# Kernel tuning notes

Hardware: AMD Instinct MI355X
Metric: run time of the kernel (lower is better)

The kernel has to match this reference:

```python
import jax, jax.numpy as jnp
import numpy as np

N = 100000   # nodes
G = 128      # graphs for mean pool


def gcn_conv(x, edge_index, W, b, num_nodes):
    # PyG GCNConv (default): x' = D^-1/2 (A+I) D^-1/2 (x W) + b
    x = x @ W
    src, dst = edge_index[0], edge_index[1]
    loop = jnp.arange(num_nodes)
    src = jnp.concatenate([src, loop])
    dst = jnp.concatenate([dst, loop])
    ones = jnp.ones(src.shape[0], x.dtype)
    deg = jax.ops.segment_sum(ones, dst, num_segments=num_nodes)
    dinv = jnp.where(deg > 0, jax.lax.rsqrt(deg), 0.0)
    norm = dinv[src] * dinv[dst]            # [E+N]
    msg = x[src] * norm[:, None]            # gather + scale
    out = jax.ops.segment_sum(msg, dst, num_segments=num_nodes)  # scatter-add
    return out + b


def setup_inputs() -> dict:
    key = jax.random.key(0)
    ks = jax.random.split(key, 5)
    x = jax.random.normal(ks[0], (N, 128), jnp.float32)
    edge_index = jax.random.randint(ks[1], (2, 1600000), 0, N)
    batch = jnp.sort(jax.random.randint(ks[2], (N,), 0, G))
    W1 = jax.random.normal(ks[3], (128, 64), jnp.float32) / np.sqrt(128.0)
    b1 = jnp.zeros((64,), jnp.float32)
    W2 = jax.random.normal(ks[4], (64, 64), jnp.float32) / np.sqrt(64.0)
    b2 = jnp.zeros((64,), jnp.float32)
    return {"x": x, "edge_index": edge_index, "batch": batch,
            "W1": W1, "b1": b1, "W2": W2, "b2": b2}


def reference(x, edge_index, batch, W1, b1, W2, b2):
    h = gcn_conv(x, edge_index, W1, b1, N)
    h = jax.nn.relu(h)  # dropout is identity in eval mode
    h = gcn_conv(h, edge_index, W2, b2, N)
    # global_mean_pool over graph ids
    s = jax.ops.segment_sum(h, batch, num_segments=G)
    cnt = jax.ops.segment_sum(jnp.ones((N,), h.dtype), batch, num_segments=G)
    return s / jnp.maximum(cnt, 1.0)[:, None]   # [G, hidden2]
```

## Files before the change

kernel.cpp:

```cpp
#include <hip/hip_runtime.h>
#include <hip/hip_fp16.h>

#define SLOTS 64
#define DEGSTRIDE 16

typedef _Float16 half8 __attribute__((ext_vector_type(8)));
typedef float f32x4 __attribute__((ext_vector_type(4)));

__global__ __launch_bounds__(256) void fill_pad(const int* __restrict__ src,
                                                const int* __restrict__ dst, int E, int N,
                                                int* __restrict__ degp,
                                                int* __restrict__ colpad, int chunks) {
  int range = blockIdx.x & 7;
  int chunk = blockIdx.x >> 3;
  int per = (N + 7) >> 3;
  int lo = range * per, hi = min(N, lo + per);
  int e0 = (int)((long long)chunk * E / chunks);
  int e1 = (int)((long long)(chunk + 1) * E / chunks);
  for (int e = e0 + (int)threadIdx.x; e < e1; e += 256) {
    int d = dst[e];
    if (d >= lo && d < hi) {
      int p = atomicAdd(&degp[(size_t)d * DEGSTRIDE], 1);
      if (p < SLOTS) colpad[(size_t)d * SLOTS + p] = src[e];
    }
  }
}

__global__ __launch_bounds__(256) void calc_dinv(const int* __restrict__ degp,
                                                 float* __restrict__ dinv,
                                                 int* __restrict__ degc, int N) {
  int i = blockIdx.x * 256 + threadIdx.x;
  if (i < N) {
    int d = degp[(size_t)i * DEGSTRIDE];
    dinv[i] = rsqrtf((float)(d + 1));
    degc[i] = min(d, SLOTS);
  }
}

template <int K, typename Tin>
__global__ __launch_bounds__(256) void gemm_mfma(const Tin* __restrict__ in,
                                                 const float* __restrict__ W,
                                                 const float* __restrict__ dinv,
                                                 __half* __restrict__ out,
                                                 int N) {
  constexpr int LDK = K + 8;
  __shared__ __align__(16) _Float16 Wt[64][LDK];
  int t = threadIdx.x;
  int wave = t >> 6, lane = t & 63;
  int arow = lane & 15, kgrp = lane >> 4;
  constexpr int KK = K / 32;
  int row0 = blockIdx.x * 64;
  int row = row0 + wave * 16 + arow;

  half8 af[KK];
  if (row < N) {
#pragma unroll
    for (int kk = 0; kk < KK; ++kk) {
      if constexpr (sizeof(Tin) == 4) {
        const float4* p = (const float4*)&in[(size_t)row * K + kk * 32 + kgrp * 8];
        float4 v0 = p[0], v1 = p[1];
        half8 h;
        h[0] = (_Float16)v0.x; h[1] = (_Float16)v0.y;
        h[2] = (_Float16)v0.z; h[3] = (_Float16)v0.w;
        h[4] = (_Float16)v1.x; h[5] = (_Float16)v1.y;
        h[6] = (_Float16)v1.z; h[7] = (_Float16)v1.w;
        af[kk] = h;
      } else {
        af[kk] = *(const half8*)&in[(size_t)row * K + kk * 32 + kgrp * 8];
      }
    }
  } else {
#pragma unroll
    for (int kk = 0; kk < KK; ++kk) af[kk] = (half8)((_Float16)0.f);
  }
  int rbase = row0 + wave * 16 + kgrp * 4;
  float dv[4];
#pragma unroll
  for (int r = 0; r < 4; ++r) dv[r] = (rbase + r < N) ? dinv[rbase + r] : 0.f;

  for (int j = t; j < K * 64; j += 256) {
    int k = j >> 6, c = j & 63;
    Wt[c][k] = (_Float16)W[j];
  }
  __syncthreads();

  f32x4 acc[4];
#pragma unroll
  for (int ct = 0; ct < 4; ++ct) acc[ct] = (f32x4)(0.f);
#pragma unroll
  for (int kk = 0; kk < KK; ++kk) {
#pragma unroll
    for (int ct = 0; ct < 4; ++ct) {
      half8 b = *(const half8*)&Wt[ct * 16 + arow][kk * 32 + kgrp * 8];
      acc[ct] = __builtin_amdgcn_mfma_f32_16x16x32_f16(af[kk], b, acc[ct], 0, 0, 0);
    }
  }

#pragma unroll
  for (int r = 0; r < 4; ++r) {
    int rr = rbase + r;
    if (rr < N) {
#pragma unroll
      for (int ct = 0; ct < 4; ++ct)
        out[(size_t)rr * 64 + ct * 16 + arow] = __float2half(acc[ct][r] * dv[r]);
    }
  }
}

__global__ __launch_bounds__(256) void aggregate(const __half* __restrict__ g,
                                                 const int* __restrict__ degc,
                                                 const int* __restrict__ colpad,
                                                 const float* __restrict__ dinv,
                                                 const float* __restrict__ bias,
                                                 const int* __restrict__ batch,
                                                 __half* __restrict__ out,
                                                 float* __restrict__ poolsum,
                                                 float* __restrict__ poolcnt,
                                                 int N, int mode) {
  int lane = threadIdx.x & 63;
  int wave = blockIdx.x * 4 + (threadIdx.x >> 6);
  int nwaves = gridDim.x * 4;
  int per = (N + nwaves - 1) / nwaves;
  int n0 = wave * per, n1 = min(N, n0 + per);
  if (n0 >= n1) return;
  float b = bias[lane];
  int cur = mode ? batch[n0] : 0;
  float pacc = 0.f, pcnt = 0.f;
  int deg = degc[n0];
  int nb = colpad[(size_t)n0 * SLOTS + lane];
  for (int node = n0; node < n1; ++node) {
    int nxt = (node + 1 < n1) ? node + 1 : node;
    int dn = degc[nxt];
    int nbn = colpad[(size_t)nxt * SLOTS + lane];
    float a0 = __half2float(g[(size_t)node * 64 + lane]);
    float a1 = 0.f, a2 = 0.f, a3 = 0.f;
    float a4 = 0.f, a5 = 0.f, a6 = 0.f, a7 = 0.f;
    int j = 0;
    for (; j + 7 < deg; j += 8) {
      int s0 = __shfl(nb, j, 64);
      int s1 = __shfl(nb, j + 1, 64);
      int s2 = __shfl(nb, j + 2, 64);
      int s3 = __shfl(nb, j + 3, 64);
      int s4 = __shfl(nb, j + 4, 64);
      int s5 = __shfl(nb, j + 5, 64);
      int s6 = __shfl(nb, j + 6, 64);
      int s7 = __shfl(nb, j + 7, 64);
      a0 += __half2float(g[(size_t)s0 * 64 + lane]);
      a1 += __half2float(g[(size_t)s1 * 64 + lane]);
      a2 += __half2float(g[(size_t)s2 * 64 + lane]);
      a3 += __half2float(g[(size_t)s3 * 64 + lane]);
      a4 += __half2float(g[(size_t)s4 * 64 + lane]);
      a5 += __half2float(g[(size_t)s5 * 64 + lane]);
      a6 += __half2float(g[(size_t)s6 * 64 + lane]);
      a7 += __half2float(g[(size_t)s7 * 64 + lane]);
    }
    for (; j + 3 < deg; j += 4) {
      int s0 = __shfl(nb, j, 64);
      int s1 = __shfl(nb, j + 1, 64);
      int s2 = __shfl(nb, j + 2, 64);
      int s3 = __shfl(nb, j + 3, 64);
      a0 += __half2float(g[(size_t)s0 * 64 + lane]);
      a1 += __half2float(g[(size_t)s1 * 64 + lane]);
      a2 += __half2float(g[(size_t)s2 * 64 + lane]);
      a3 += __half2float(g[(size_t)s3 * 64 + lane]);
    }
    for (; j < deg; ++j) a0 += __half2float(g[(size_t)__shfl(nb, j, 64) * 64 + lane]);
    float r = dinv[node] * (((a0 + a1) + (a2 + a3)) + ((a4 + a5) + (a6 + a7))) + b;
    deg = dn;
    nb = nbn;
    if (mode == 0) {
      out[(size_t)node * 64 + lane] = __float2half(fmaxf(r, 0.f));
    } else {
      int bg = batch[node];
      if (bg != cur) {
        atomicAdd(&poolsum[cur * 64 + lane], pacc);
        if (lane == 0) atomicAdd(&poolcnt[cur], pcnt);
        pacc = 0.f; pcnt = 0.f; cur = bg;
      }
      pacc += r; pcnt += 1.f;
    }
  }
  if (mode) {
    atomicAdd(&poolsum[cur * 64 + lane], pacc);
    if (lane == 0) atomicAdd(&poolcnt[cur], pcnt);
  }
}

__global__ __launch_bounds__(256) void finalize(const float* __restrict__ poolsum,
                                                const float* __restrict__ poolcnt,
                                                float* __restrict__ out, int Gn) {
  int i = blockIdx.x * 256 + threadIdx.x;
  if (i < Gn * 64) {
    float c = poolcnt[i >> 6];
    out[i] = poolsum[i] / fmaxf(c, 1.f);
  }
}

extern "C" void kernel_launch(void* const* d_in, const int* in_sizes, int n_in,
                              void* d_out, int out_size, void* d_ws, size_t ws_size,
                              hipStream_t stream) {
  const float* x   = (const float*)d_in[0];
  const int* ei    = (const int*)d_in[1];
  const int* batch = (const int*)d_in[2];
  const float* W1  = (const float*)d_in[3];
  const float* b1  = (const float*)d_in[4];
  const float* W2  = (const float*)d_in[5];
  const float* b2  = (const float*)d_in[6];
  float* out = (float*)d_out;

  int N  = in_sizes[2];
  int E  = in_sizes[1] / 2;
  int Gn = out_size / 64;

  char* ws = (char*)d_ws;
  size_t off = 0;
  auto alloc = [&](size_t bytes) -> void* {
    void* p = ws + off;
    off = (off + bytes + 255) & ~(size_t)255;
    return p;
  };
  float* poolsum = (float*)alloc(4ull * Gn * 64);
  float* poolcnt = (float*)alloc(4ull * Gn);
  size_t zero_bytes = off;
  int* colpad    = (int*)alloc(4ull * (size_t)N * SLOTS);
  float* dinv    = (float*)alloc(4ull * N);
  int* degc      = (int*)alloc(4ull * N);
  __half* gbuf   = (__half*)alloc(2ull * (size_t)N * 64);
  __half* ybuf   = (__half*)alloc(2ull * (size_t)N * 64);
  int* degp = (int*)gbuf;
  (void)ws_size; (void)n_in;

  hipMemsetAsync(poolsum, 0, zero_bytes, stream);
  hipMemsetAsync(degp, 0, 4ull * (size_t)N * DEGSTRIDE, stream);

  const int* srcv = ei;
  const int* dstv = ei + E;
  int tiles64 = (N + 63) / 64;

  fill_pad<<<8 * 256, 256, 0, stream>>>(srcv, dstv, E, N, degp, colpad, 256);
  calc_dinv<<<(N + 255) / 256, 256, 0, stream>>>(degp, dinv, degc, N);

  gemm_mfma<128, float><<<tiles64, 256, 0, stream>>>(x, W1, dinv, gbuf, N);
  aggregate<<<2048, 256, 0, stream>>>(gbuf, degc, colpad, dinv, b1, batch, ybuf,
                                      nullptr, nullptr, N, 0);
  gemm_mfma<64, __half><<<tiles64, 256, 0, stream>>>(ybuf, W2, dinv, gbuf, N);
  aggregate<<<2048, 256, 0, stream>>>(gbuf, degc, colpad, dinv, b2, batch, nullptr,
                                      poolsum, poolcnt, N, 1);
  finalize<<<(Gn * 64 + 255) / 256, 256, 0, stream>>>(poolsum, poolcnt, out, Gn);
}
```

Measured before the change: 307.0 us.

## Run edge bucketing and first GEMM in one launch, apply degree scaling afterward

Merges the CSR-padding fill kernel and the first layer's MFMA GEMM into one grid, with block ranges selecting the role, so the atomic-bound fill and the bandwidth-bound GEMM can overlap. Since dinv is not yet known during the GEMM, a new elementwise kernel computes dinv/degc from the counts and rescales the GEMM output in place. The degree counters move to the second buffer to avoid aliasing the GEMM output. This adds an extra read/write pass over the N×64 fp16 features and an extra fp16 rounding before scaling.

```diff
diff --git a/kernel.cpp b/kernel.cpp
--- a/kernel.cpp
+++ b/kernel.cpp
@@ -7,42 +7,114 @@
 typedef _Float16 half8 __attribute__((ext_vector_type(8)));
 typedef float f32x4 __attribute__((ext_vector_type(4)));
 
-__global__ __launch_bounds__(256) void fill_pad(const int* __restrict__ src,
-                                                const int* __restrict__ dst, int E, int N,
-                                                int* __restrict__ degp,
-                                                int* __restrict__ colpad, int chunks) {
-  int range = blockIdx.x & 7;
-  int chunk = blockIdx.x >> 3;
-  int per = (N + 7) >> 3;
-  int lo = range * per, hi = min(N, lo + per);
-  int e0 = (int)((long long)chunk * E / chunks);
-  int e1 = (int)((long long)(chunk + 1) * E / chunks);
-  for (int e = e0 + (int)threadIdx.x; e < e1; e += 256) {
-    int d = dst[e];
-    if (d >= lo && d < hi) {
-      int p = atomicAdd(&degp[(size_t)d * DEGSTRIDE], 1);
-      if (p < SLOTS) colpad[(size_t)d * SLOTS + p] = src[e];
-    }
-  }
-}
-
-__global__ __launch_bounds__(256) void calc_dinv(const int* __restrict__ degp,
-                                                 float* __restrict__ dinv,
-                                                 int* __restrict__ degc, int N) {
-  int i = blockIdx.x * 256 + threadIdx.x;
-  if (i < N) {
-    int d = degp[(size_t)i * DEGSTRIDE];
-    dinv[i] = rsqrtf((float)(d + 1));
-    degc[i] = min(d, SLOTS);
-  }
-}
-
-template <int K, typename Tin>
-__global__ __launch_bounds__(256) void gemm_mfma(const Tin* __restrict__ in,
-                                                 const float* __restrict__ W,
-                                                 const float* __restrict__ dinv,
-                                                 __half* __restrict__ out,
-                                                 int N) {
+__global__ __launch_bounds__(256) void fused_fill_gemm(
+    const int* __restrict__ src, const int* __restrict__ dst, int E, int N,
+    int* __restrict__ degp, int* __restrict__ colpad, int chunks,
+    const float* __restrict__ in, const float* __restrict__ W,
+    __half* __restrict__ out, int tiles) {
+  constexpr int K = 128;
+  constexpr int LDK = K + 8;
+  __shared__ __align__(16) _Float16 Wt[64][LDK];
+  int bid = blockIdx.x;
+
+  if (bid < 8 * chunks) {
+    int range = bid & 7;
+    int chunk = bid >> 3;
+    int per = (N + 7) >> 3;
+    int lo = range * per, hi = min(N, lo + per);
+    int e0 = (int)((long long)chunk * E / chunks);
+    int e1 = (int)((long long)(chunk + 1) * E / chunks);
+    for (int e = e0 + (int)threadIdx.x; e < e1; e += 256) {
+      int d = dst[e];
+      if (d >= lo && d < hi) {
+        int p = atomicAdd(&degp[(size_t)d * DEGSTRIDE], 1);
+        if (p < SLOTS) colpad[(size_t)d * SLOTS + p] = src[e];
+      }
+    }
+    return;
+  }
+
+  int tile = bid - 8 * chunks;
+  if (tile >= tiles) return;
+  int t = threadIdx.x;
+  int wave = t >> 6, lane = t & 63;
+  int arow = lane & 15, kgrp = lane >> 4;
+  constexpr int KK = K / 32;
+  int row0 = tile * 64;
+  int row = row0 + wave * 16 + arow;
+
+  half8 af[KK];
+  if (row < N) {
+#pragma unroll
+    for (int kk = 0; kk < KK; ++kk) {
+      const float4* p = (const float4*)&in[(size_t)row * K + kk * 32 + kgrp * 8];
+      float4 v0 = p[0], v1 = p[1];
+      half8 h;
+      h[0] = (_Float16)v0.x; h[1] = (_Float16)v0.y;
+      h[2] = (_Float16)v0.z; h[3] = (_Float16)v0.w;
+      h[4] = (_Float16)v1.x; h[5] = (_Float16)v1.y;
+      h[6] = (_Float16)v1.z; h[7] = (_Float16)v1.w;
+      af[kk] = h;
+    }
+  } else {
+#pragma unroll
+    for (int kk = 0; kk < KK; ++kk) af[kk] = (half8)((_Float16)0.f);
+  }
+
+  for (int j = t; j < K * 64; j += 256) {
+    int k = j >> 6, c = j & 63;
+    Wt[c][k] = (_Float16)W[j];
+  }
+  __syncthreads();
+
+  f32x4 acc[4];
+#pragma unroll
+  for (int ct = 0; ct < 4; ++ct) acc[ct] = (f32x4)(0.f);
+#pragma unroll
+  for (int kk = 0; kk < KK; ++kk) {
+#pragma unroll
+    for (int ct = 0; ct < 4; ++ct) {
+      half8 b = *(const half8*)&Wt[ct * 16 + arow][kk * 32 + kgrp * 8];
+      acc[ct] = __builtin_amdgcn_mfma_f32_16x16x32_f16(af[kk], b, acc[ct], 0, 0, 0);
+    }
+  }
+
+  int rbase = row0 + wave * 16 + kgrp * 4;
+#pragma unroll
+  for (int r = 0; r < 4; ++r) {
+    int rr = rbase + r;
+    if (rr < N) {
+#pragma unroll
+      for (int ct = 0; ct < 4; ++ct)
+        out[(size_t)rr * 64 + ct * 16 + arow] = __float2half(acc[ct][r]);
+    }
+  }
+}
+
+__global__ __launch_bounds__(256) void scale_dinv(const int* __restrict__ degp,
+                                                  __half* __restrict__ g,
+                                                  float* __restrict__ dinv,
+                                                  int* __restrict__ degc, int N) {
+  int idx = blockIdx.x * 256 + threadIdx.x;
+  if (idx >= N * 8) return;
+  int row = idx >> 3;
+  int d = degp[(size_t)row * DEGSTRIDE];
+  float s = rsqrtf((float)(d + 1));
+  half8 h = *(half8*)&g[(size_t)idx * 8];
+#pragma unroll
+  for (int j = 0; j < 8; ++j) h[j] = (_Float16)((float)h[j] * s);
+  *(half8*)&g[(size_t)idx * 8] = h;
+  if ((idx & 7) == 0) {
+    dinv[row] = s;
+    degc[row] = min(d, SLOTS);
+  }
+}
+
+__global__ __launch_bounds__(256) void gemm_mfma64(const __half* __restrict__ in,
+                                                   const float* __restrict__ W,
+                                                   const float* __restrict__ dinv,
+                                                   __half* __restrict__ out, int N) {
+  constexpr int K = 64;
   constexpr int LDK = K + 8;
   __shared__ __align__(16) _Float16 Wt[64][LDK];
   int t = threadIdx.x;
@@ -55,20 +127,8 @@
   half8 af[KK];
   if (row < N) {
 #pragma unroll
-    for (int kk = 0; kk < KK; ++kk) {
-      if constexpr (sizeof(Tin) == 4) {
-        const float4* p = (const float4*)&in[(size_t)row * K + kk * 32 + kgrp * 8];
-        float4 v0 = p[0], v1 = p[1];
-        half8 h;
-        h[0] = (_Float16)v0.x; h[1] = (_Float16)v0.y;
-        h[2] = (_Float16)v0.z; h[3] = (_Float16)v0.w;
-        h[4] = (_Float16)v1.x; h[5] = (_Float16)v1.y;
-        h[6] = (_Float16)v1.z; h[7] = (_Float16)v1.w;
-        af[kk] = h;
-      } else {
-        af[kk] = *(const half8*)&in[(size_t)row * K + kk * 32 + kgrp * 8];
-      }
-    }
+    for (int kk = 0; kk < KK; ++kk)
+      af[kk] = *(const half8*)&in[(size_t)row * K + kk * 32 + kgrp * 8];
   } else {
 #pragma unroll
     for (int kk = 0; kk < KK; ++kk) af[kk] = (half8)((_Float16)0.f);
@@ -95,7 +155,6 @@
       acc[ct] = __builtin_amdgcn_mfma_f32_16x16x32_f16(af[kk], b, acc[ct], 0, 0, 0);
     }
   }
-
 #pragma unroll
   for (int r = 0; r < 4; ++r) {
     int rr = rbase + r;
@@ -227,7 +286,7 @@
   int* degc      = (int*)alloc(4ull * N);
   __half* gbuf   = (__half*)alloc(2ull * (size_t)N * 64);
   __half* ybuf   = (__half*)alloc(2ull * (size_t)N * 64);
-  int* degp = (int*)gbuf;
+  int* degp = (int*)ybuf;
   (void)ws_size; (void)n_in;
 
   hipMemsetAsync(poolsum, 0, zero_bytes, stream);
@@ -236,14 +295,15 @@
   const int* srcv = ei;
   const int* dstv = ei + E;
   int tiles64 = (N + 63) / 64;
-
-  fill_pad<<<8 * 256, 256, 0, stream>>>(srcv, dstv, E, N, degp, colpad, 256);
-  calc_dinv<<<(N + 255) / 256, 256, 0, stream>>>(degp, dinv, degc, N);
-
-  gemm_mfma<128, float><<<tiles64, 256, 0, stream>>>(x, W1, dinv, gbuf, N);
+  int chunks = 256;
+
+  fused_fill_gemm<<<8 * chunks + tiles64, 256, 0, stream>>>(
+      srcv, dstv, E, N, degp, colpad, chunks, x, W1, gbuf, tiles64);
+  scale_dinv<<<(N * 8 + 255) / 256, 256, 0, stream>>>(degp, gbuf, dinv, degc, N);
+
   aggregate<<<2048, 256, 0, stream>>>(gbuf, degc, colpad, dinv, b1, batch, ybuf,
                                       nullptr, nullptr, N, 0);
-  gemm_mfma<64, __half><<<tiles64, 256, 0, stream>>>(ybuf, W2, dinv, gbuf, N);
+  gemm_mfma64<<<tiles64, 256, 0, stream>>>(ybuf, W2, dinv, gbuf, N);
   aggregate<<<2048, 256, 0, stream>>>(gbuf, degc, colpad, dinv, b2, batch, nullptr,
                                       poolsum, poolcnt, N, 1);
   finalize<<<(Gn * 64 + 255) / 256, 256, 0, stream>>>(poolsum, poolcnt, out, Gn);
```

Result: no change. 308.3 us (+0.4%).
